# Kernel tuning notes

Measured on AMD Instinct MI355X. Metric: run time of the kernel, lower is better.

The kernel has to match this reference:

```python
import jax, jax.numpy as jnp
import numpy as np

NEG_INF_FILL = -1000000.0  # matches torch code's masked fill value


def setup_inputs() -> dict:
    key = jax.random.key(0)
    kK, kV, kQ, kL = jax.random.split(key, 4)
    B, Sq, Sk, d, dv = 8, 2048, 2048, 512, 512
    return {
        "K": jax.random.normal(kK, (B, Sk, d), dtype=jnp.float32),
        "V": jax.random.normal(kV, (B, Sk, dv), dtype=jnp.float32),
        "Q": jax.random.normal(kQ, (B, Sq, d), dtype=jnp.float32),
        "valid_len": jax.random.randint(kL, (Sq,), 0, dv, dtype=jnp.int64),
    }


def reference(K, V, Q, valid_len):
    d = K.shape[-1]
    # score: [B, Sq, Sk]
    score = jnp.einsum("bqd,bkd->bqk", Q, K) / jnp.sqrt(jnp.asarray(d, Q.dtype))
    # x: [B, Sq, dv] -- NOTE: original applies mask+softmax to score @ V
    x = jnp.einsum("bqk,bkv->bqv", score, V)
    dv = x.shape[-1]
    # mask rows: per-query-position valid_len compared to feature index 0..dv-1
    mask = jnp.arange(dv)[None, :] > valid_len[:, None]  # [Sq, dv]
    x = jnp.where(mask[None, :, :], jnp.asarray(NEG_INF_FILL, x.dtype), x)
    return jax.nn.softmax(x, axis=-1)
```

## Files before the change

kernel.cpp:

```cpp
#include <hip/hip_runtime.h>
#include <hip/hip_bf16.h>
#include <math.h>

#define BATCH 8
#define SQ 2048
#define SK 2048
#define DD 512
#define DV 512
#define RP 40

typedef short bf16x8_t __attribute__((ext_vector_type(8)));
typedef float f32x4_t __attribute__((ext_vector_type(4)));

__device__ __forceinline__ unsigned int pk_bf16(float a, float b) {
    __hip_bfloat162 h = __float22bfloat162_rn(float2{a, b});
    unsigned int u;
    __builtin_memcpy(&u, &h, 4);
    return u;
}
__device__ __forceinline__ float from_hi(unsigned int u) {
    return __builtin_bit_cast(float, u);
}

__global__ __launch_bounds__(256) void ktv_mfma(const float* __restrict__ Kp,
                                                const float* __restrict__ Vp,
                                                float* __restrict__ Mpart) {
    const int b  = blockIdx.z & 7;
    const int ts = blockIdx.z >> 3;
    const int d0 = blockIdx.x * 128;
    const int v0 = blockIdx.y * 128;
    const float* Kb = Kp + (size_t)b * SK * DD;
    const float* Vb = Vp + (size_t)b * SK * DV;

    __shared__ __align__(16) unsigned short Kh[128 * RP], Kl[128 * RP],
                                            Vh[128 * RP], Vl[128 * RP];

    const int tid  = threadIdx.x;
    const int lane = tid & 63;
    const int w    = tid >> 6;
    const int wv   = (w & 1) * 64;
    const int wd   = (w >> 1) * 64;
    const int uu   = tid >> 5;
    const int xx   = tid & 31;

    f32x4_t acc[4][4];
#pragma unroll
    for (int i = 0; i < 4; ++i)
#pragma unroll
        for (int j = 0; j < 4; ++j) acc[i][j] = (f32x4_t){0.f, 0.f, 0.f, 0.f};

    const int tb = ts * 512;

    float kr0[2][4], kr1[2][4], vr0[2][4], vr1[2][4];
    auto load_tile = [&](int t0l) {
#pragma unroll
        for (int p = 0; p < 2; ++p) {
            const int t = 16 * p + 2 * uu;
            const size_t gr = (size_t)(tb + t0l + t);
#pragma unroll
            for (int c = 0; c < 4; ++c) {
                const int d = xx + 32 * c;
                kr0[p][c] = Kb[gr * DD + d0 + d];
                kr1[p][c] = Kb[(gr + 1) * DD + d0 + d];
                vr0[p][c] = Vb[gr * DV + v0 + d];
                vr1[p][c] = Vb[(gr + 1) * DV + v0 + d];
            }
        }
    };

    load_tile(0);
    for (int t0 = 0; t0 < 512; t0 += 32) {
#pragma unroll
        for (int p = 0; p < 2; ++p) {
            const int t  = 16 * p + 2 * uu;
            const int to = (t >> 3) * 8 + (t & 7);
#pragma unroll
            for (int c = 0; c < 4; ++c) {
                const int d   = xx + 32 * c;
                const int off = d * RP + to;
                {
                    const unsigned int h = pk_bf16(kr0[p][c], kr1[p][c]);
                    const float r0 = kr0[p][c] - from_hi(h << 16);
                    const float r1 = kr1[p][c] - from_hi(h & 0xFFFF0000u);
                    *(unsigned int*)(Kh + off) = h;
                    *(unsigned int*)(Kl + off) = pk_bf16(r0, r1);
                }
                {
                    const unsigned int h = pk_bf16(vr0[p][c], vr1[p][c]);
                    const float r0 = vr0[p][c] - from_hi(h << 16);
                    const float r1 = vr1[p][c] - from_hi(h & 0xFFFF0000u);
                    *(unsigned int*)(Vh + off) = h;
                    *(unsigned int*)(Vl + off) = pk_bf16(r0, r1);
                }
            }
        }
        __syncthreads();

        if (t0 + 32 < 512) load_tile(t0 + 32);

        const int kq = lane >> 4;
        const int mr = lane & 15;
        bf16x8_t ah[4], al_[4];
#pragma unroll
        for (int tm = 0; tm < 4; ++tm) {
            const int off = (wv + tm * 16 + mr) * RP + kq * 8;
            ah[tm]  = *(const bf16x8_t*)(Vh + off);
            al_[tm] = *(const bf16x8_t*)(Vl + off);
        }
#pragma unroll
        for (int tn = 0; tn < 4; ++tn) {
            const int off = (wd + tn * 16 + mr) * RP + kq * 8;
            const bf16x8_t bh = *(const bf16x8_t*)(Kh + off);
            const bf16x8_t bl = *(const bf16x8_t*)(Kl + off);
#pragma unroll
            for (int tm = 0; tm < 4; ++tm) {
                acc[tm][tn] = __builtin_amdgcn_mfma_f32_16x16x32_bf16(ah[tm], bh, acc[tm][tn], 0, 0, 0);
                acc[tm][tn] = __builtin_amdgcn_mfma_f32_16x16x32_bf16(ah[tm], bl, acc[tm][tn], 0, 0, 0);
                acc[tm][tn] = __builtin_amdgcn_mfma_f32_16x16x32_bf16(al_[tm], bh, acc[tm][tn], 0, 0, 0);
            }
        }
        __syncthreads();
    }

    float* Mp = Mpart + (size_t)(ts * 8 + b) * DV * DD;
    const int quad = lane >> 4;
    const int col  = lane & 15;
#pragma unroll
    for (int tm = 0; tm < 4; ++tm)
#pragma unroll
        for (int tn = 0; tn < 4; ++tn)
#pragma unroll
            for (int r = 0; r < 4; ++r) {
                const int v = v0 + wv + tm * 16 + quad * 4 + r;
                const int d = d0 + wd + tn * 16 + col;
                Mp[(size_t)v * DD + d] = acc[tm][tn][r];
            }
}

__global__ __launch_bounds__(256) void reduce_cvt(const float* __restrict__ Mpart,
                                                  unsigned short* __restrict__ Mth,
                                                  unsigned short* __restrict__ Mtl) {
    const size_t N  = (size_t)BATCH * DD * DV;
    const size_t i4 = ((size_t)blockIdx.x * 256 + threadIdx.x) * 4;

    float sx = 0.f, sy = 0.f, sz = 0.f, sw = 0.f;
#pragma unroll
    for (int sl = 0; sl < 4; ++sl) {
        const float4 f = *(const float4*)&Mpart[sl * N + i4];
        sx += f.x; sy += f.y; sz += f.z; sw += f.w;
    }

    const float s = 0.04419417382415922f;
    const float m0 = sx * s, m1 = sy * s, m2 = sz * s, m3 = sw * s;
    const unsigned int h0 = pk_bf16(m0, m1);
    const unsigned int h1 = pk_bf16(m2, m3);
    const float r0 = m0 - from_hi(h0 << 16);
    const float r1 = m1 - from_hi(h0 & 0xFFFF0000u);
    const float r2 = m2 - from_hi(h1 << 16);
    const float r3 = m3 - from_hi(h1 & 0xFFFF0000u);
    *(uint2*)&Mth[i4] = make_uint2(h0, h1);
    *(uint2*)&Mtl[i4] = make_uint2(pk_bf16(r0, r1), pk_bf16(r2, r3));
}

__global__ __launch_bounds__(256) void qm_mfma(const float* __restrict__ Qp,
                                               const unsigned short* __restrict__ Mth,
                                               const unsigned short* __restrict__ Mtl,
                                               float* __restrict__ Xp) {
    const int b  = blockIdx.z;
    const int q0 = blockIdx.x * 128;
    const int v0 = blockIdx.y * 128;
    const float* Qb = Qp + (size_t)b * SQ * DD;
    const unsigned short* Bhg = Mth + (size_t)b * DV * DD;
    const unsigned short* Blg = Mtl + (size_t)b * DV * DD;

    __shared__ __align__(16) unsigned short Qh[128 * RP], Ql[128 * RP],
                                            Bh[128 * RP], Bl[128 * RP];

    const int tid  = threadIdx.x;
    const int lane = tid & 63;
    const int w    = tid >> 6;
    const int wq   = (w & 1) * 64;
    const int wv   = (w >> 1) * 64;

    f32x4_t acc[4][4];
#pragma unroll
    for (int i = 0; i < 4; ++i)
#pragma unroll
        for (int j = 0; j < 4; ++j) acc[i][j] = (f32x4_t){0.f, 0.f, 0.f, 0.f};

    float4 pq[4];
    bf16x8_t pbh[2], pbl[2];
    const int qrow = tid >> 3;
    const int qdc  = (tid & 7) * 4;
    const int brow = tid >> 2;
    const int bkq  = tid & 3;
    auto load_tile = [&](int k0l) {
#pragma unroll
        for (int p = 0; p < 4; ++p)
            pq[p] = *(const float4*)&Qb[(size_t)(q0 + p * 32 + qrow) * DD + k0l + qdc];
#pragma unroll
        for (int p = 0; p < 2; ++p) {
            const size_t go = (size_t)(v0 + p * 64 + brow) * DD + k0l + bkq * 8;
            pbh[p] = *(const bf16x8_t*)&Bhg[go];
            pbl[p] = *(const bf16x8_t*)&Blg[go];
        }
    };

    load_tile(0);
    for (int k0 = 0; k0 < DD; k0 += 32) {
#pragma unroll
        for (int p = 0; p < 4; ++p) {
            const float4 f = pq[p];
            const unsigned int h01 = pk_bf16(f.x, f.y);
            const unsigned int h23 = pk_bf16(f.z, f.w);
            const float r0 = f.x - from_hi(h01 << 16);
            const float r1 = f.y - from_hi(h01 & 0xFFFF0000u);
            const float r2 = f.z - from_hi(h23 << 16);
            const float r3 = f.w - from_hi(h23 & 0xFFFF0000u);
            const int off = (p * 32 + qrow) * RP + qdc;
            *(uint2*)(Qh + off) = make_uint2(h01, h23);
            *(uint2*)(Ql + off) = make_uint2(pk_bf16(r0, r1), pk_bf16(r2, r3));
        }
#pragma unroll
        for (int p = 0; p < 2; ++p) {
            const int off = (p * 64 + brow) * RP + bkq * 8;
            *(bf16x8_t*)(Bh + off) = pbh[p];
            *(bf16x8_t*)(Bl + off) = pbl[p];
        }
        __syncthreads();

        if (k0 + 32 < DD) load_tile(k0 + 32);

        const int kq = lane >> 4;
        const int mr = lane & 15;
        bf16x8_t ah[4], al_[4];
#pragma unroll
        for (int tm = 0; tm < 4; ++tm) {
            const int off = (wq + tm * 16 + mr) * RP + kq * 8;
            ah[tm]  = *(const bf16x8_t*)(Qh + off);
            al_[tm] = *(const bf16x8_t*)(Ql + off);
        }
#pragma unroll
        for (int tn = 0; tn < 4; ++tn) {
            const int off = (wv + tn * 16 + mr) * RP + kq * 8;
            const bf16x8_t bh = *(const bf16x8_t*)(Bh + off);
            const bf16x8_t bl = *(const bf16x8_t*)(Bl + off);
#pragma unroll
            for (int tm = 0; tm < 4; ++tm) {
                acc[tm][tn] = __builtin_amdgcn_mfma_f32_16x16x32_bf16(ah[tm], bh, acc[tm][tn], 0, 0, 0);
                acc[tm][tn] = __builtin_amdgcn_mfma_f32_16x16x32_bf16(ah[tm], bl, acc[tm][tn], 0, 0, 0);
                acc[tm][tn] = __builtin_amdgcn_mfma_f32_16x16x32_bf16(al_[tm], bh, acc[tm][tn], 0, 0, 0);
            }
        }
        __syncthreads();
    }

    float* Xb = Xp + (size_t)b * SQ * DV;
    const int quad = lane >> 4;
    const int col  = lane & 15;
#pragma unroll
    for (int tm = 0; tm < 4; ++tm)
#pragma unroll
        for (int tn = 0; tn < 4; ++tn)
#pragma unroll
            for (int r = 0; r < 4; ++r)
                Xb[(size_t)(q0 + wq + tm * 16 + quad * 4 + r) * DV + v0 + wv + tn * 16 + col] = acc[tm][tn][r];
}

__global__ __launch_bounds__(256) void softmax_kernel(float* __restrict__ X,
                                                      const int* __restrict__ vlen) {
    const int wave = threadIdx.x >> 6;
    const int lane = threadIdx.x & 63;
    const int row  = blockIdx.x * 4 + wave;
    const int q    = row & (SQ - 1);
    float* xr = X + (size_t)row * DV;
    const int vl = vlen[q];

    float v[8];
#pragma unroll
    for (int u = 0; u < 2; ++u) {
        const int j0 = u * 256 + lane * 4;
        const float4 f = *(const float4*)&xr[j0];
        v[u * 4 + 0] = (j0 + 0 > vl) ? -1.0e6f : f.x;
        v[u * 4 + 1] = (j0 + 1 > vl) ? -1.0e6f : f.y;
        v[u * 4 + 2] = (j0 + 2 > vl) ? -1.0e6f : f.z;
        v[u * 4 + 3] = (j0 + 3 > vl) ? -1.0e6f : f.w;
    }

    float m = v[0];
#pragma unroll
    for (int i = 1; i < 8; ++i) m = fmaxf(m, v[i]);
#pragma unroll
    for (int off = 32; off > 0; off >>= 1) m = fmaxf(m, __shfl_xor(m, off, 64));

    float ssum = 0.f;
#pragma unroll
    for (int i = 0; i < 8; ++i) {
        v[i] = __expf(v[i] - m);
        ssum += v[i];
    }
#pragma unroll
    for (int off = 32; off > 0; off >>= 1) ssum += __shfl_xor(ssum, off, 64);

    const float inv = 1.0f / ssum;
#pragma unroll
    for (int u = 0; u < 2; ++u) {
        const int j0 = u * 256 + lane * 4;
        float4 o;
        o.x = v[u * 4 + 0] * inv;
        o.y = v[u * 4 + 1] * inv;
        o.z = v[u * 4 + 2] * inv;
        o.w = v[u * 4 + 3] * inv;
        *(float4*)&xr[j0] = o;
    }
}

extern "C" void kernel_launch(void* const* d_in, const int* in_sizes, int n_in,
                              void* d_out, int out_size, void* d_ws, size_t ws_size,
                              hipStream_t stream) {
    const float* Kp   = (const float*)d_in[0];
    const float* Vp   = (const float*)d_in[1];
    const float* Qp   = (const float*)d_in[2];
    const int*   vlen = (const int*)d_in[3];
    float* out = (float*)d_out;

    unsigned short* Mth = (unsigned short*)d_ws;
    unsigned short* Mtl = Mth + (size_t)BATCH * DD * DV;
    float* Mpart = out;

    ktv_mfma<<<dim3(4, 4, 32), 256, 0, stream>>>(Kp, Vp, Mpart);
    reduce_cvt<<<dim3(2048), 256, 0, stream>>>(Mpart, Mth, Mtl);
    qm_mfma<<<dim3(16, 4, 8), 256, 0, stream>>>(Qp, Mth, Mtl, out);
    softmax_kernel<<<dim3(BATCH * SQ / 4), 256, 0, stream>>>(out, vlen);
}
```

Before: 194.8 us.

## Fuse masked softmax into Q·M GEMM with full-row tiles per block

Merges the Q×M GEMM and the separate masked-softmax kernel into one kernel. Each 512-thread block now computes a 64-query by 512-column tile, so whole rows are resident. The mask, max and sum are then reduced across waves through shared memory before the output is written once. This removes the write and re-read of the 32MB intermediate X plus one launch. In exchange the grid shrinks to 256 blocks and the B tile in LDS grows, which lowers occupancy and Q reuse.

```diff
diff --git a/kernel.cpp b/kernel.cpp
--- a/kernel.cpp
+++ b/kernel.cpp
@@ -162,25 +162,27 @@
     *(uint2*)&Mtl[i4] = make_uint2(pk_bf16(r0, r1), pk_bf16(r2, r3));
 }
 
-__global__ __launch_bounds__(256) void qm_mfma(const float* __restrict__ Qp,
-                                               const unsigned short* __restrict__ Mth,
-                                               const unsigned short* __restrict__ Mtl,
-                                               float* __restrict__ Xp) {
+__global__ __launch_bounds__(512) void qmsm(const float* __restrict__ Qp,
+                                            const unsigned short* __restrict__ Mth,
+                                            const unsigned short* __restrict__ Mtl,
+                                            const int* __restrict__ vlen,
+                                            float* __restrict__ Xp) {
     const int b  = blockIdx.z;
-    const int q0 = blockIdx.x * 128;
-    const int v0 = blockIdx.y * 128;
+    const int q0 = blockIdx.x * 64;
     const float* Qb = Qp + (size_t)b * SQ * DD;
     const unsigned short* Bhg = Mth + (size_t)b * DV * DD;
     const unsigned short* Blg = Mtl + (size_t)b * DV * DD;
 
-    __shared__ __align__(16) unsigned short Qh[128 * RP], Ql[128 * RP],
-                                            Bh[128 * RP], Bl[128 * RP];
+    __shared__ __align__(16) unsigned short Qh[64 * RP], Ql[64 * RP],
+                                            Bh[512 * RP], Bl[512 * RP];
+    __shared__ float red_m[8][64], red_s[8][64];
+    __shared__ int vls[64];
 
     const int tid  = threadIdx.x;
     const int lane = tid & 63;
     const int w    = tid >> 6;
-    const int wq   = (w & 1) * 64;
-    const int wv   = (w >> 1) * 64;
+
+    if (tid < 64) vls[tid] = vlen[q0 + tid];
 
     f32x4_t acc[4][4];
 #pragma unroll
@@ -188,19 +190,18 @@
 #pragma unroll
         for (int j = 0; j < 4; ++j) acc[i][j] = (f32x4_t){0.f, 0.f, 0.f, 0.f};
 
-    float4 pq[4];
-    bf16x8_t pbh[2], pbl[2];
     const int qrow = tid >> 3;
     const int qdc  = (tid & 7) * 4;
-    const int brow = tid >> 2;
+    const int br   = tid >> 2;
     const int bkq  = tid & 3;
+
+    float4 pq;
+    bf16x8_t pbh[4], pbl[4];
     auto load_tile = [&](int k0l) {
-#pragma unroll
-        for (int p = 0; p < 4; ++p)
-            pq[p] = *(const float4*)&Qb[(size_t)(q0 + p * 32 + qrow) * DD + k0l + qdc];
-#pragma unroll
-        for (int p = 0; p < 2; ++p) {
-            const size_t go = (size_t)(v0 + p * 64 + brow) * DD + k0l + bkq * 8;
+        pq = *(const float4*)&Qb[(size_t)(q0 + qrow) * DD + k0l + qdc];
+#pragma unroll
+        for (int p = 0; p < 4; ++p) {
+            const size_t go = (size_t)(p * 128 + br) * DD + k0l + bkq * 8;
             pbh[p] = *(const bf16x8_t*)&Bhg[go];
             pbl[p] = *(const bf16x8_t*)&Blg[go];
         }
@@ -208,22 +209,21 @@
 
     load_tile(0);
     for (int k0 = 0; k0 < DD; k0 += 32) {
-#pragma unroll
-        for (int p = 0; p < 4; ++p) {
-            const float4 f = pq[p];
+        {
+            const float4 f = pq;
             const unsigned int h01 = pk_bf16(f.x, f.y);
             const unsigned int h23 = pk_bf16(f.z, f.w);
             const float r0 = f.x - from_hi(h01 << 16);
             const float r1 = f.y - from_hi(h01 & 0xFFFF0000u);
             const float r2 = f.z - from_hi(h23 << 16);
             const float r3 = f.w - from_hi(h23 & 0xFFFF0000u);
-            const int off = (p * 32 + qrow) * RP + qdc;
+            const int off = qrow * RP + qdc;
             *(uint2*)(Qh + off) = make_uint2(h01, h23);
             *(uint2*)(Ql + off) = make_uint2(pk_bf16(r0, r1), pk_bf16(r2, r3));
         }
 #pragma unroll
-        for (int p = 0; p < 2; ++p) {
-            const int off = (p * 64 + brow) * RP + bkq * 8;
+        for (int p = 0; p < 4; ++p) {
+            const int off = (p * 128 + br) * RP + bkq * 8;
             *(bf16x8_t*)(Bh + off) = pbh[p];
             *(bf16x8_t*)(Bl + off) = pbl[p];
         }
@@ -236,13 +236,13 @@
         bf16x8_t ah[4], al_[4];
 #pragma unroll
         for (int tm = 0; tm < 4; ++tm) {
-            const int off = (wq + tm * 16 + mr) * RP + kq * 8;
+            const int off = (tm * 16 + mr) * RP + kq * 8;
             ah[tm]  = *(const bf16x8_t*)(Qh + off);
             al_[tm] = *(const bf16x8_t*)(Ql + off);
         }
 #pragma unroll
         for (int tn = 0; tn < 4; ++tn) {
-            const int off = (wv + tn * 16 + mr) * RP + kq * 8;
+            const int off = (w * 64 + tn * 16 + mr) * RP + kq * 8;
             const bf16x8_t bh = *(const bf16x8_t*)(Bh + off);
             const bf16x8_t bl = *(const bf16x8_t*)(Bl + off);
 #pragma unroll
@@ -255,64 +255,92 @@
         __syncthreads();
     }
 
-    float* Xb = Xp + (size_t)b * SQ * DV;
     const int quad = lane >> 4;
     const int col  = lane & 15;
-#pragma unroll
-    for (int tm = 0; tm < 4; ++tm)
-#pragma unroll
-        for (int tn = 0; tn < 4; ++tn)
+
+#pragma unroll
+    for (int tm = 0; tm < 4; ++tm)
+#pragma unroll
+        for (int r = 0; r < 4; ++r) {
+            const int vl = vls[tm * 16 + quad * 4 + r];
+#pragma unroll
+            for (int tn = 0; tn < 4; ++tn) {
+                const int v = w * 64 + tn * 16 + col;
+                if (v > vl) acc[tm][tn][r] = -1.0e6f;
+            }
+        }
+
+    float pm[4][4];
+#pragma unroll
+    for (int tm = 0; tm < 4; ++tm)
+#pragma unroll
+        for (int r = 0; r < 4; ++r) {
+            float m = acc[tm][0][r];
+#pragma unroll
+            for (int tn = 1; tn < 4; ++tn) m = fmaxf(m, acc[tm][tn][r]);
+#pragma unroll
+            for (int off = 1; off < 16; off <<= 1) m = fmaxf(m, __shfl_xor(m, off, 64));
+            pm[tm][r] = m;
+        }
+    if (col == 0) {
+#pragma unroll
+        for (int tm = 0; tm < 4; ++tm)
 #pragma unroll
             for (int r = 0; r < 4; ++r)
-                Xb[(size_t)(q0 + wq + tm * 16 + quad * 4 + r) * DV + v0 + wv + tn * 16 + col] = acc[tm][tn][r];
-}
-
-__global__ __launch_bounds__(256) void softmax_kernel(float* __restrict__ X,
-                                                      const int* __restrict__ vlen) {
-    const int wave = threadIdx.x >> 6;
-    const int lane = threadIdx.x & 63;
-    const int row  = blockIdx.x * 4 + wave;
-    const int q    = row & (SQ - 1);
-    float* xr = X + (size_t)row * DV;
-    const int vl = vlen[q];
-
-    float v[8];
-#pragma unroll
-    for (int u = 0; u < 2; ++u) {
-        const int j0 = u * 256 + lane * 4;
-        const float4 f = *(const float4*)&xr[j0];
-        v[u * 4 + 0] = (j0 + 0 > vl) ? -1.0e6f : f.x;
-        v[u * 4 + 1] = (j0 + 1 > vl) ? -1.0e6f : f.y;
-        v[u * 4 + 2] = (j0 + 2 > vl) ? -1.0e6f : f.z;
-        v[u * 4 + 3] = (j0 + 3 > vl) ? -1.0e6f : f.w;
-    }
-
-    float m = v[0];
-#pragma unroll
-    for (int i = 1; i < 8; ++i) m = fmaxf(m, v[i]);
-#pragma unroll
-    for (int off = 32; off > 0; off >>= 1) m = fmaxf(m, __shfl_xor(m, off, 64));
-
-    float ssum = 0.f;
-#pragma unroll
-    for (int i = 0; i < 8; ++i) {
-        v[i] = __expf(v[i] - m);
-        ssum += v[i];
-    }
-#pragma unroll
-    for (int off = 32; off > 0; off >>= 1) ssum += __shfl_xor(ssum, off, 64);
-
-    const float inv = 1.0f / ssum;
-#pragma unroll
-    for (int u = 0; u < 2; ++u) {
-        const int j0 = u * 256 + lane * 4;
-        float4 o;
-        o.x = v[u * 4 + 0] * inv;
-        o.y = v[u * 4 + 1] * inv;
-        o.z = v[u * 4 + 2] * inv;
-        o.w = v[u * 4 + 3] * inv;
-        *(float4*)&xr[j0] = o;
-    }
+                red_m[w][tm * 16 + quad * 4 + r] = pm[tm][r];
+    }
+    __syncthreads();
+
+    float rm[4][4];
+#pragma unroll
+    for (int tm = 0; tm < 4; ++tm)
+#pragma unroll
+        for (int r = 0; r < 4; ++r) {
+            const int row = tm * 16 + quad * 4 + r;
+            float m = red_m[0][row];
+#pragma unroll
+            for (int w2 = 1; w2 < 8; ++w2) m = fmaxf(m, red_m[w2][row]);
+            rm[tm][r] = m;
+        }
+
+#pragma unroll
+    for (int tm = 0; tm < 4; ++tm)
+#pragma unroll
+        for (int r = 0; r < 4; ++r) {
+            float s = 0.f;
+#pragma unroll
+            for (int tn = 0; tn < 4; ++tn) {
+                const float p = __expf(acc[tm][tn][r] - rm[tm][r]);
+                acc[tm][tn][r] = p;
+                s += p;
+            }
+#pragma unroll
+            for (int off = 1; off < 16; off <<= 1) s += __shfl_xor(s, off, 64);
+            pm[tm][r] = s;
+        }
+    if (col == 0) {
+#pragma unroll
+        for (int tm = 0; tm < 4; ++tm)
+#pragma unroll
+            for (int r = 0; r < 4; ++r)
+                red_s[w][tm * 16 + quad * 4 + r] = pm[tm][r];
+    }
+    __syncthreads();
+
+    float* Xb = Xp + (size_t)b * SQ * DV;
+#pragma unroll
+    for (int tm = 0; tm < 4; ++tm)
+#pragma unroll
+        for (int r = 0; r < 4; ++r) {
+            const int row = tm * 16 + quad * 4 + r;
+            float s = red_s[0][row];
+#pragma unroll
+            for (int w2 = 1; w2 < 8; ++w2) s += red_s[w2][row];
+            const float inv = 1.0f / s;
+#pragma unroll
+            for (int tn = 0; tn < 4; ++tn)
+                Xb[(size_t)(q0 + row) * DV + w * 64 + tn * 16 + col] = acc[tm][tn][r] * inv;
+        }
 }
 
 extern "C" void kernel_launch(void* const* d_in, const int* in_sizes, int n_in,
@@ -330,6 +358,5 @@
 
     ktv_mfma<<<dim3(4, 4, 32), 256, 0, stream>>>(Kp, Vp, Mpart);
     reduce_cvt<<<dim3(2048), 256, 0, stream>>>(Mpart, Mth, Mtl);
-    qm_mfma<<<dim3(16, 4, 8), 256, 0, stream>>>(Qp, Mth, Mtl, out);
-    softmax_kernel<<<dim3(BATCH * SQ / 4), 256, 0, stream>>>(out, vlen);
-}
+    qmsm<<<dim3(32, 1, 8), 512, 0, stream>>>(Qp, Mth, Mtl, vlen, out);
+}
```

Result: slower. 201.6 us (+3.5%).
